# Optimization experiments

Hardware: AMD Instinct MI355X
Metric: run time of the kernel (lower is better)

## Reference

```python
import jax, jax.numpy as jnp
import numpy as np

E = 512
H = 8
D = E // H
HID = 2048
NE = 4
TOPK = 2
EPS = 1e-5
NEG = -1e9


def _ln(x, w, b):
    mu = jnp.mean(x, axis=-1, keepdims=True)
    var = jnp.mean(jnp.square(x - mu), axis=-1, keepdims=True)
    return (x - mu) * jax.lax.rsqrt(var + EPS) * w + b


def _expert(xf, mask, ln1_w, ln1_b, ipw, ipb, opw, opb, ln2_w, ln2_b, w1, b1, w2, b2):
    # xf: [T, E]; mask: [T] bool (allowed keys = routed tokens)
    T = xf.shape[0]
    h = _ln(xf, ln1_w, ln1_b)
    qkv = h @ ipw.T + ipb                       # [T, 3E]
    q, k, v = jnp.split(qkv, 3, axis=-1)
    q = q.reshape(T, H, D).transpose(1, 0, 2)   # [H, T, D]
    k = k.reshape(T, H, D).transpose(1, 0, 2)
    v = v.reshape(T, H, D).transpose(1, 0, 2)
    scores = jnp.einsum('htd,hsd->hts', q, k) / jnp.sqrt(jnp.asarray(D, xf.dtype))
    scores = jnp.where(mask[None, None, :], scores, NEG)
    a = jax.nn.softmax(scores, axis=-1)
    o = jnp.einsum('hts,hsd->htd', a, v).transpose(1, 0, 2).reshape(T, E)
    o = o @ opw.T + opb
    x1 = xf + o                                 # residual (dropout = identity, eval)
    h2 = _ln(x1, ln2_w, ln2_b)
    m = jax.nn.gelu(h2 @ w1.T + b1, approximate=False) @ w2.T + b2
    return x1 + m


def setup_inputs() -> dict:
    key = jax.random.key(0)
    ks = jax.random.split(key, 16)
    s = 0.02
    inp = {
        'x': jax.random.normal(ks[0], (4, 512, E), dtype=jnp.float32),
        'gate_w': jax.random.normal(ks[1], (NE, E), dtype=jnp.float32) * s,
        'gate_b': jnp.zeros((NE,), jnp.float32),
        'ln1_w': jnp.ones((NE, E), jnp.float32),
        'ln1_b': jnp.zeros((NE, E), jnp.float32),
        'in_proj_w': jax.random.normal(ks[2], (NE, 3 * E, E), dtype=jnp.float32) * s,
        'in_proj_b': jnp.zeros((NE, 3 * E), jnp.float32),
        'out_proj_w': jax.random.normal(ks[3], (NE, E, E), dtype=jnp.float32) * s,
        'out_proj_b': jnp.zeros((NE, E), jnp.float32),
        'ln2_w': jnp.ones((NE, E), jnp.float32),
        'ln2_b': jnp.zeros((NE, E), jnp.float32),
        'mlp_w1': jax.random.normal(ks[4], (NE, HID, E), dtype=jnp.float32) * s,
        'mlp_b1': jnp.zeros((NE, HID), jnp.float32),
        'mlp_w2': jax.random.normal(ks[5], (NE, E, HID), dtype=jnp.float32) * s,
        'mlp_b2': jnp.zeros((NE, E), jnp.float32),
    }
    return inp


def reference(x, gate_w, gate_b, ln1_w, ln1_b, in_proj_w, in_proj_b, out_proj_w,
              out_proj_b, ln2_w, ln2_b, mlp_w1, mlp_b1, mlp_w2, mlp_b2):
    B, N, _ = x.shape
    T = B * N
    xf = x.reshape(T, E)
    logits = xf @ gate_w.T + gate_b                      # [T, NE]
    topk_val, topk_idx = jax.lax.top_k(logits, TOPK)
    probs = jax.nn.softmax(topk_val, axis=-1)            # [T, TOPK]
    out = jnp.zeros_like(xf)
    for kk in range(TOPK):
        idx = topk_idx[:, kk]
        w = probs[:, kk][:, None]
        for e in range(NE):
            mask = idx == e
            eo = _expert(xf, mask,
                         ln1_w[e], ln1_b[e], in_proj_w[e], in_proj_b[e],
                         out_proj_w[e], out_proj_b[e], ln2_w[e], ln2_b[e],
                         mlp_w1[e], mlp_b1[e], mlp_w2[e], mlp_b2[e])
            out = out + jnp.where(mask[:, None], eo * w, 0.0)
    return out.reshape(B, N, E)
```

## Files before the change

### kernel.cpp

```cpp
#include <hip/hip_runtime.h>
#include <hip/hip_bf16.h>

#define T_TOK 2048
#define E_DIM 512
#define NHEAD 8
#define DHEAD 64
#define HID_D 2048
#define NEXP 4
#define NROW_ (2 * T_TOK)
#define VT_STRIDE 4352

typedef short short8 __attribute__((ext_vector_type(8)));
typedef float floatx4 __attribute__((ext_vector_type(4)));

__device__ __forceinline__ void gld16(const void* g, void* l) {
  __builtin_amdgcn_global_load_lds((const __attribute__((address_space(1))) void*)g,
                                   (__attribute__((address_space(3))) void*)l, 16, 0, 0);
}

__device__ inline float wave_sum(float v) {
  for (int off = 32; off > 0; off >>= 1) v += __shfl_xor(v, off);
  return v;
}

__device__ __forceinline__ unsigned pack_bf2(float a, float b) {
  __hip_bfloat16 ha = __float2bfloat16(a), hb = __float2bfloat16(b);
  unsigned ua = *(unsigned short*)&ha, ub = *(unsigned short*)&hb;
  return ua | (ub << 16);
}

__device__ __forceinline__ void cvt4(const float* __restrict__ s, __hip_bfloat16* __restrict__ d,
                                     int i4, int n) {
  if (i4 < n) {
    float4 v = *reinterpret_cast<const float4*>(s + i4);
    __hip_bfloat16 tmp[4] = {__float2bfloat16(v.x), __float2bfloat16(v.y),
                             __float2bfloat16(v.z), __float2bfloat16(v.w)};
    *reinterpret_cast<ushort4*>(d + i4) = *reinterpret_cast<const ushort4*>(tmp);
  }
}

__global__ void cvt_weights(const float* __restrict__ s0, const float* __restrict__ s1,
                            const float* __restrict__ s2, const float* __restrict__ s3,
                            __hip_bfloat16* d0, __hip_bfloat16* d1,
                            __hip_bfloat16* d2, __hip_bfloat16* d3,
                            int n0, int n1, int n2, int n3) {
  int i4 = (blockIdx.x * 256 + threadIdx.x) * 4;
  cvt4(s0, d0, i4, n0);
  cvt4(s1, d1, i4, n1);
  cvt4(s2, d2, i4, n2);
  cvt4(s3, d3, i4, n3);
}

__global__ void gate_kernel(const float* __restrict__ x, const float* __restrict__ gw,
                            const float* __restrict__ gb, int* token_e, float* token_p) {
  int wid = threadIdx.x >> 6, lane = threadIdx.x & 63;
  int t = blockIdx.x * 4 + wid;
  float a0 = 0, a1 = 0, a2 = 0, a3 = 0;
  for (int i = 0; i < 8; i++) {
    int c = lane + 64 * i;
    float xv = x[(size_t)t * E_DIM + c];
    a0 += xv * gw[0 * E_DIM + c];
    a1 += xv * gw[1 * E_DIM + c];
    a2 += xv * gw[2 * E_DIM + c];
    a3 += xv * gw[3 * E_DIM + c];
  }
  a0 = wave_sum(a0); a1 = wave_sum(a1); a2 = wave_sum(a2); a3 = wave_sum(a3);
  if (lane == 0) {
    float lg[4] = {a0 + gb[0], a1 + gb[1], a2 + gb[2], a3 + gb[3]};
    int i0 = 0;
    for (int e = 1; e < 4; e++) if (lg[e] > lg[i0]) i0 = e;
    int i1 = -1;
    for (int e = 0; e < 4; e++) {
      if (e == i0) continue;
      if (i1 < 0 || lg[e] > lg[i1]) i1 = e;
    }
    float e1 = __expf(lg[i1] - lg[i0]);
    float inv = 1.f / (1.f + e1);
    token_e[t] = i0; token_e[T_TOK + t] = i1;
    token_p[t] = inv; token_p[T_TOK + t] = e1 * inv;
  }
}

__global__ void count_kernel(const int* __restrict__ token_e, int* counts) {
  int g = blockIdx.x, kk = g >> 2, e = g & 3;
  __shared__ int ws4[4];
  int tid = threadIdx.x, wid = tid >> 6, lane = tid & 63;
  int c = 0;
  for (int t = tid; t < T_TOK; t += 256) c += (token_e[kk * T_TOK + t] == e);
  for (int off = 32; off; off >>= 1) c += __shfl_xor(c, off);
  if (lane == 0) ws4[wid] = c;
  __syncthreads();
  if (tid == 0) counts[g] = ws4[0] + ws4[1] + ws4[2] + ws4[3];
}

__global__ void offs_kernel(const int* __restrict__ counts, int* offs, int* padoffs) {
  int o = 0, po = 0;
  offs[0] = 0; padoffs[0] = 0;
  for (int g = 0; g < 8; g++) {
    o += counts[g]; offs[g + 1] = o;
    po += (counts[g] + 31) & ~31; padoffs[g + 1] = po;
  }
}

__global__ void compact_kernel(const int* __restrict__ token_e, const int* __restrict__ offs,
                               const int* __restrict__ padoffs, int* perm, int* rowg,
                               int* pmap, int* invrow) {
  int g = blockIdx.x, kk = g >> 2, e = g & 3;
  __shared__ int wcnt[4];
  __shared__ int base;
  int tid = threadIdx.x, wid = tid >> 6, lane = tid & 63;
  int og = offs[g], pg = padoffs[g];
  if (tid == 0) base = 0;
  __syncthreads();
  for (int t0 = 0; t0 < T_TOK; t0 += 256) {
    int t = t0 + tid;
    bool pred = token_e[kk * T_TOK + t] == e;
    unsigned long long mask = __ballot(pred);
    int rank = __popcll(mask & ((1ull << lane) - 1ull));
    if (lane == 0) wcnt[wid] = __popcll(mask);
    __syncthreads();
    int woff = 0;
    for (int i = 0; i < wid; i++) woff += wcnt[i];
    if (pred) {
      int row = og + base + woff + rank;
      perm[row] = t;
      rowg[row] = g;
      pmap[row] = pg + (row - og);
      invrow[kk * T_TOK + t] = row;
    }
    __syncthreads();
    if (tid == 0) base += wcnt[0] + wcnt[1] + wcnt[2] + wcnt[3];
    __syncthreads();
  }
}

__global__ void ln_kernel(const float* __restrict__ src, const int* __restrict__ perm,
                          const int* __restrict__ rowg, const float* __restrict__ lnw,
                          const float* __restrict__ lnb, __hip_bfloat16* __restrict__ dst) {
  int wid = threadIdx.x >> 6, lane = threadIdx.x & 63;
  int row = blockIdx.x * 4 + wid;
  int e = rowg[row] & 3;
  const float* xr = src + (size_t)(perm ? perm[row] : row) * E_DIM;
  float v[8];
  float s = 0;
  for (int i = 0; i < 8; i++) { v[i] = xr[lane + 64 * i]; s += v[i]; }
  s = wave_sum(s);
  float mu = s * (1.f / 512.f);
  float q = 0;
  for (int i = 0; i < 8; i++) { float d = v[i] - mu; q += d * d; }
  q = wave_sum(q);
  float rstd = rsqrtf(q * (1.f / 512.f) + 1e-5f);
  for (int i = 0; i < 8; i++) {
    int c = lane + 64 * i;
    dst[(size_t)row * E_DIM + c] =
        __float2bfloat16((v[i] - mu) * rstd * lnw[e * E_DIM + c] + lnb[e * E_DIM + c]);
  }
}

__global__ void transpose_v(const short* __restrict__ v, const int* __restrict__ pmap,
                            short* __restrict__ vT) {
  __shared__ short tile[64][65];
  int r0 = blockIdx.x * 64, c0 = blockIdx.y * 64;
  int tc = threadIdx.x & 63, tr4 = threadIdx.x >> 6;
  for (int i = 0; i < 64; i += 4)
    tile[tr4 + i][tc] = v[(size_t)(r0 + tr4 + i) * E_DIM + c0 + tc];
  __syncthreads();
  int pcol = pmap[r0 + tc];
  for (int i = 0; i < 64; i += 4)
    vT[(size_t)(c0 + tr4 + i) * VT_STRIDE + pcol] = tile[tc][tr4 + i];
}

__global__ void zero_gaps(const int* __restrict__ offs, const int* __restrict__ padoffs,
                          short* __restrict__ vT) {
  int g = blockIdx.x;
  int cnt = offs[g + 1] - offs[g];
  int gap = (padoffs[g + 1] - padoffs[g]) - cnt;
  if ((int)threadIdx.x < gap) {
    int col = padoffs[g] + cnt + threadIdx.x;
    for (int d = blockIdx.y; d < E_DIM; d += gridDim.y)
      vT[(size_t)d * VT_STRIDE + col] = 0;
  }
}

__global__ __launch_bounds__(256) void attn_mfma(
    const short* __restrict__ qb, const short* __restrict__ kb,
    const short* __restrict__ vT, const int* __restrict__ offs,
    const int* __restrict__ padoffs, __hip_bfloat16* __restrict__ ob) {
  int d0 = blockIdx.x;
  int g = d0 & 7;
  int rem = d0 >> 3;
  int h = rem >> 5;
  int qblk = rem & 31;
  int sbeg = offs[g], rend = offs[g + 1];
  int q0 = sbeg + qblk * 64;
  if (q0 >= rend) return;
  int G = rend - sbeg;
  int pg = padoffs[g];
  int tid = threadIdx.x, wid = tid >> 6, lane = tid & 63;
  int fr = lane & 15, lg = lane >> 4;
  int qw = q0 + wid * 16;

  __shared__ short Kt[2][32 * 64];
  __shared__ short Vt[2][64 * 32];

  int arow = qw + fr; if (arow > rend - 1) arow = rend - 1;
  const short* qp = qb + (size_t)arow * E_DIM + h * DHEAD;
  short8 qf0 = *reinterpret_cast<const short8*>(qp + lg * 8);
  short8 qf1 = *reinterpret_cast<const short8*>(qp + 32 + lg * 8);

  int offB = tid * 16;
  int krow = offB >> 7, kinner = offB & 127;
  int ksrc = (kinner ^ ((krow & 7) << 4)) >> 1;
  int vL = offB ^ (((offB >> 7) & 7) << 4);
  int vd = vL >> 6, vkey0 = (vL & 63) >> 1;
  int wb = wid * 512;
  const short* vrow = vT + (size_t)(h * DHEAD + vd) * VT_STRIDE + pg;

  auto stage = [&](int buf, int kbase) {
    int gr = sbeg + kbase + krow; if (gr > NROW_ - 1) gr = NROW_ - 1;
    gld16(kb + (size_t)gr * E_DIM + h * DHEAD + ksrc, &Kt[buf][wb]);
    gld16(vrow + kbase + vkey0, &Vt[buf][wb]);
  };

  floatx4 acc[4] = {};
  float m_r = -1e30f, l_r = 0.f;

  stage(0, 0);
  asm volatile("s_waitcnt vmcnt(0)" ::: "memory");
  __syncthreads();

  int cur = 0;
  for (int kbase = 0; kbase < G; kbase += 32) {
    if (kbase + 32 < G) stage(cur ^ 1, kbase + 32);
    const char* Kb = (const char*)&Kt[cur][0];
    const char* Vb = (const char*)&Vt[cur][0];

    int r0r = fr, r1r = 16 + fr;
    short8 kf00 = *reinterpret_cast<const short8*>(Kb + r0r * 128 + ((lg * 16) ^ ((r0r & 7) << 4)));
    short8 kf01 = *reinterpret_cast<const short8*>(Kb + r0r * 128 + ((64 + lg * 16) ^ ((r0r & 7) << 4)));
    short8 kf10 = *reinterpret_cast<const short8*>(Kb + r1r * 128 + ((lg * 16) ^ ((r1r & 7) << 4)));
    short8 kf11 = *reinterpret_cast<const short8*>(Kb + r1r * 128 + ((64 + lg * 16) ^ ((r1r & 7) << 4)));

    floatx4 s0 = {}, s1 = {};
    s0 = __builtin_amdgcn_mfma_f32_16x16x32_bf16(kf00, qf0, s0, 0, 0, 0);
    s0 = __builtin_amdgcn_mfma_f32_16x16x32_bf16(kf01, qf1, s0, 0, 0, 0);
    s1 = __builtin_amdgcn_mfma_f32_16x16x32_bf16(kf10, qf0, s1, 0, 0, 0);
    s1 = __builtin_amdgcn_mfma_f32_16x16x32_bf16(kf11, qf1, s1, 0, 0, 0);

    float sv[8];
    float mloc = -1e30f;
#pragma unroll
    for (int j = 0; j < 4; j++) {
      int k0 = kbase + lg * 4 + j;
      sv[j] = (k0 < G) ? s0[j] * 0.125f : -1e30f;
      sv[4 + j] = (k0 + 16 < G) ? s1[j] * 0.125f : -1e30f;
      mloc = fmaxf(mloc, fmaxf(sv[j], sv[4 + j]));
    }
    mloc = fmaxf(mloc, __shfl_xor(mloc, 16));
    mloc = fmaxf(mloc, __shfl_xor(mloc, 32));
    if (__any(mloc > m_r + 8.f)) {
      float mn = fmaxf(m_r, mloc);
      float corr = __expf(m_r - mn);
      m_r = mn;
      l_r *= corr;
      float cq0 = __shfl(corr, lg * 4 + 0), cq1 = __shfl(corr, lg * 4 + 1);
      float cq2 = __shfl(corr, lg * 4 + 2), cq3 = __shfl(corr, lg * 4 + 3);
#pragma unroll
      for (int db = 0; db < 4; db++) {
        acc[db][0] *= cq0; acc[db][1] *= cq1; acc[db][2] *= cq2; acc[db][3] *= cq3;
      }
    }
    float p[8], sl = 0.f;
#pragma unroll
    for (int i = 0; i < 8; i++) { p[i] = __expf(sv[i] - m_r); sl += p[i]; }
    sl += __shfl_xor(sl, 16);
    sl += __shfl_xor(sl, 32);
    l_r += sl;

    union { unsigned u[4]; short8 s8; } pa0, pa1;
    pa0.u[0] = pack_bf2(p[0], p[1]); pa0.u[1] = pack_bf2(p[2], p[3]);
    pa0.u[2] = 0; pa0.u[3] = 0;
    pa1.u[0] = pack_bf2(p[4], p[5]); pa1.u[1] = pack_bf2(p[6], p[7]);
    pa1.u[2] = 0; pa1.u[3] = 0;

#pragma unroll
    for (int db = 0; db < 4; db++) {
      int dd = db * 16 + fr;
      int s = ((dd >> 1) & 7) << 4;
      uint2 w0 = *reinterpret_cast<const uint2*>(Vb + ((dd * 64 + lg * 8) ^ s));
      uint2 w1 = *reinterpret_cast<const uint2*>(Vb + ((dd * 64 + 32 + lg * 8) ^ s));
      union { unsigned u[4]; short8 s8; } bv0, bv1;
      bv0.u[0] = w0.x; bv0.u[1] = w0.y; bv0.u[2] = 0; bv0.u[3] = 0;
      bv1.u[0] = w1.x; bv1.u[1] = w1.y; bv1.u[2] = 0; bv1.u[3] = 0;
      acc[db] = __builtin_amdgcn_mfma_f32_16x16x32_bf16(pa0.s8, bv0.s8, acc[db], 0, 0, 0);
      acc[db] = __builtin_amdgcn_mfma_f32_16x16x32_bf16(pa1.s8, bv1.s8, acc[db], 0, 0, 0);
    }

    asm volatile("s_waitcnt vmcnt(0)" ::: "memory");
    __syncthreads();
    cur ^= 1;
  }

  float lq0 = __shfl(l_r, lg * 4 + 0), lq1 = __shfl(l_r, lg * 4 + 1);
  float lq2 = __shfl(l_r, lg * 4 + 2), lq3 = __shfl(l_r, lg * 4 + 3);
  float lq[4] = {lq0, lq1, lq2, lq3};
#pragma unroll
  for (int db = 0; db < 4; db++)
#pragma unroll
    for (int j = 0; j < 4; j++) {
      int row = qw + lg * 4 + j;
      if (row < rend)
        ob[(size_t)row * E_DIM + h * DHEAD + db * 16 + fr] = __float2bfloat16(acc[db][j] / lq[j]);
    }
}

template <int MODE>
__global__ __launch_bounds__(256) void gemm_mfma(
    const short* __restrict__ A, const short* __restrict__ Wb,
    const float* __restrict__ bias, const int* __restrict__ offs,
    const int* __restrict__ perm, const float* __restrict__ resid,
    __hip_bfloat16* __restrict__ bq, __hip_bfloat16* __restrict__ bk,
    __hip_bfloat16* __restrict__ bv, float* __restrict__ outf) {
  constexpr int K = (MODE == 3) ? HID_D : E_DIM;
  constexpr int N = (MODE == 0) ? 3 * E_DIM : (MODE == 2) ? HID_D : E_DIM;
  constexpr int NKSTEP = K / 64;
  constexpr int NXB = 32;
  __shared__ short Abuf[2][4096];
  __shared__ short Bbuf[2][4096];

  int d = blockIdx.x;
  int g = d & 7;
  int rem = d >> 3;
  int yb = rem / NXB, xb = rem % NXB;
  int e = g & 3;
  int rbeg = offs[g], rend = offs[g + 1];
  int row0 = rbeg + xb * 64;
  if (row0 >= rend) return;
  int col0 = yb * 64;
  int tid = threadIdx.x;
  int wid = tid >> 6, lane = tid & 63;
  int wm = wid >> 1, wn = wid & 1;
  int fr = lane & 15, lg = lane >> 4;
  const short* wbase = Wb + (size_t)e * N * K;

  int st_row[2], st_src[2], st_arow[2];
  int wavebase = wid << 9;
  for (int c = 0; c < 2; c++) {
    int off = c * 4096 + tid * 16;
    int trow = off >> 7;
    int inner = off & 127;
    st_row[c] = trow;
    st_src[c] = (inner ^ ((trow & 7) << 4)) >> 1;
    int ga = row0 + trow;
    st_arow[c] = ga < rend ? ga : rend - 1;
  }

  auto stage = [&](int buf, int kb) {
#pragma unroll
    for (int c = 0; c < 2; c++) {
      gld16(A + (size_t)st_arow[c] * K + kb + st_src[c], &Abuf[buf][c * 2048 + wavebase]);
      gld16(wbase + (size_t)(col0 + st_row[c]) * K + kb + st_src[c],
            &Bbuf[buf][c * 2048 + wavebase]);
    }
  };

  floatx4 acc[2][2] = {};
  stage(0, 0);
  asm volatile("s_waitcnt vmcnt(0)" ::: "memory");
  __syncthreads();

  int cur = 0;
  for (int t = 0; t < NKSTEP; ++t) {
    if (t + 1 < NKSTEP) stage(cur ^ 1, (t + 1) * 64);
    const char* Ab = (const char*)&Abuf[cur][0];
    const char* Bb = (const char*)&Bbuf[cur][0];
    short8 af[2][2], bf8[2][2];
#pragma unroll
    for (int mi = 0; mi < 2; mi++)
#pragma unroll
      for (int ks = 0; ks < 2; ks++) {
        int row = wm * 32 + mi * 16 + fr;
        int cb = ks * 64 + lg * 16;
        af[mi][ks] = *reinterpret_cast<const short8*>(Ab + row * 128 + (cb ^ ((row & 7) << 4)));
      }
#pragma unroll
    for (int ni = 0; ni < 2; ni++)
#pragma unroll
      for (int ks = 0; ks < 2; ks++) {
        int row = wn * 32 + ni * 16 + fr;
        int cb = ks * 64 + lg * 16;
        bf8[ni][ks] = *reinterpret_cast<const short8*>(Bb + row * 128 + (cb ^ ((row & 7) << 4)));
      }
#pragma unroll
    for (int mi = 0; mi < 2; mi++)
#pragma unroll
      for (int ni = 0; ni < 2; ni++) {
        acc[mi][ni] = __builtin_amdgcn_mfma_f32_16x16x32_bf16(af[mi][0], bf8[ni][0], acc[mi][ni], 0, 0, 0);
        acc[mi][ni] = __builtin_amdgcn_mfma_f32_16x16x32_bf16(af[mi][1], bf8[ni][1], acc[mi][ni], 0, 0, 0);
      }
    asm volatile("s_waitcnt vmcnt(0)" ::: "memory");
    __syncthreads();
    cur ^= 1;
  }

  for (int mi = 0; mi < 2; mi++)
    for (int ni = 0; ni < 2; ni++)
      for (int j = 0; j < 4; j++) {
        int row = row0 + wm * 32 + mi * 16 + lg * 4 + j;
        if (row >= rend) continue;
        int col = col0 + wn * 32 + ni * 16 + fr;
        float val = acc[mi][ni][j] + bias[e * N + col];
        if constexpr (MODE == 0) {
          if (col < E_DIM) bq[(size_t)row * E_DIM + col] = __float2bfloat16(val);
          else if (col < 2 * E_DIM) bk[(size_t)row * E_DIM + col - E_DIM] = __float2bfloat16(val);
          else bv[(size_t)row * E_DIM + col - 2 * E_DIM] = __float2bfloat16(val);
        } else if constexpr (MODE == 1) {
          int t = perm[row];
          outf[(size_t)row * E_DIM + col] = val + resid[(size_t)t * E_DIM + col];
        } else if constexpr (MODE == 2) {
          float gl = 0.5f * val * (1.f + erff(val * 0.70710678118654752f));
          bq[(size_t)row * HID_D + col] = __float2bfloat16(gl);
        } else {
          outf[(size_t)row * E_DIM + col] = val + resid[(size_t)row * E_DIM + col];
        }
      }
}

__global__ void combine_kernel(const float* __restrict__ y, const int* __restrict__ invrow,
                               const float* __restrict__ token_p, float* __restrict__ out) {
  int t = blockIdx.x;
  int r0 = invrow[t], r1 = invrow[T_TOK + t];
  float p0 = token_p[t], p1 = token_p[T_TOK + t];
  const float* y0 = y + (size_t)r0 * E_DIM;
  const float* y1 = y + (size_t)r1 * E_DIM;
  float* o = out + (size_t)t * E_DIM;
  for (int i = threadIdx.x; i < E_DIM; i += 256) o[i] = p0 * y0[i] + p1 * y1[i];
}

extern "C" void kernel_launch(void* const* d_in, const int* in_sizes, int n_in,
                              void* d_out, int out_size, void* d_ws, size_t ws_size,
                              hipStream_t stream) {
  const float* x      = (const float*)d_in[0];
  const float* gate_w = (const float*)d_in[1];
  const float* gate_b = (const float*)d_in[2];
  const float* ln1_w  = (const float*)d_in[3];
  const float* ln1_b  = (const float*)d_in[4];
  const float* ipw    = (const float*)d_in[5];
  const float* ipb    = (const float*)d_in[6];
  const float* opw    = (const float*)d_in[7];
  const float* opb    = (const float*)d_in[8];
  const float* ln2_w  = (const float*)d_in[9];
  const float* ln2_b  = (const float*)d_in[10];
  const float* w1     = (const float*)d_in[11];
  const float* b1     = (const float*)d_in[12];
  const float* w2     = (const float*)d_in[13];
  const float* b2     = (const float*)d_in[14];
  float* out = (float*)d_out;

  const int SZ_IP = NEXP * 3 * E_DIM * E_DIM;
  const int SZ_OP = NEXP * E_DIM * E_DIM;
  const int SZ_W1 = NEXP * HID_D * E_DIM;
  const int SZ_W2 = NEXP * E_DIM * HID_D;
  const int NROW = NROW_;

  char* ws = (char*)d_ws;
  size_t off = 0;
  auto carve = [&](size_t bytes) -> void* {
    void* p = ws + off;
    off += (bytes + 255) & ~(size_t)255;
    return p;
  };
  __hip_bfloat16* ipw_bf = (__hip_bfloat16*)carve((size_t)SZ_IP * 2);
  __hip_bfloat16* opw_bf = (__hip_bfloat16*)carve((size_t)SZ_OP * 2);
  __hip_bfloat16* w1_bf  = (__hip_bfloat16*)carve((size_t)SZ_W1 * 2);
  __hip_bfloat16* w2_bf  = (__hip_bfloat16*)carve((size_t)SZ_W2 * 2);
  __hip_bfloat16* h_bf   = (__hip_bfloat16*)carve((size_t)NROW * E_DIM * 2);
  __hip_bfloat16* q_bf   = (__hip_bfloat16*)carve((size_t)NROW * E_DIM * 2);
  __hip_bfloat16* k_bf   = (__hip_bfloat16*)carve((size_t)NROW * E_DIM * 2);
  __hip_bfloat16* v_bf   = (__hip_bfloat16*)carve((size_t)NROW * E_DIM * 2);
  __hip_bfloat16* o_bf   = (__hip_bfloat16*)carve((size_t)NROW * E_DIM * 2);
  __hip_bfloat16* h2_bf  = (__hip_bfloat16*)carve((size_t)NROW * E_DIM * 2);
  __hip_bfloat16* mid_bf = (__hip_bfloat16*)carve((size_t)NROW * HID_D * 2);
  short* vT     = (short*)carve((size_t)E_DIM * VT_STRIDE * 2);
  float* x1     = (float*)carve((size_t)NROW * E_DIM * 4);
  int* token_e  = (int*)carve((size_t)NROW * 4);
  float* token_p= (float*)carve((size_t)NROW * 4);
  int* perm     = (int*)carve((size_t)NROW * 4);
  int* rowg     = (int*)carve((size_t)NROW * 4);
  int* pmap     = (int*)carve((size_t)NROW * 4);
  int* invrow   = (int*)carve((size_t)NROW * 4);
  int* counts   = (int*)carve(8 * 4);
  int* offs     = (int*)carve(9 * 4);
  int* padoffs  = (int*)carve(9 * 4);
  float* ybuf = (float*)h_bf;

  cvt_weights<<<SZ_W1 / 4 / 256, 256, 0, stream>>>(ipw, opw, w1, w2, ipw_bf, opw_bf,
                                                   w1_bf, w2_bf, SZ_IP, SZ_OP, SZ_W1, SZ_W2);
  gate_kernel<<<T_TOK / 4, 256, 0, stream>>>(x, gate_w, gate_b, token_e, token_p);
  count_kernel<<<8, 256, 0, stream>>>(token_e, counts);
  offs_kernel<<<1, 1, 0, stream>>>(counts, offs, padoffs);
  compact_kernel<<<8, 256, 0, stream>>>(token_e, offs, padoffs, perm, rowg, pmap, invrow);
  ln_kernel<<<NROW / 4, 256, 0, stream>>>(x, perm, rowg, ln1_w, ln1_b, h_bf);
  gemm_mfma<0><<<8 * 24 * 32, 256, 0, stream>>>((const short*)h_bf, (const short*)ipw_bf,
      ipb, offs, perm, nullptr, q_bf, k_bf, v_bf, nullptr);
  transpose_v<<<dim3(NROW / 64, E_DIM / 64), 256, 0, stream>>>((const short*)v_bf, pmap, vT);
  zero_gaps<<<dim3(8, 64), 32, 0, stream>>>(offs, padoffs, vT);
  attn_mfma<<<8 * 8 * 32, 256, 0, stream>>>((const short*)q_bf, (const short*)k_bf,
      vT, offs, padoffs, o_bf);
  gemm_mfma<1><<<8 * 8 * 32, 256, 0, stream>>>((const short*)o_bf, (const short*)opw_bf,
      opb, offs, perm, x, nullptr, nullptr, nullptr, x1);
  ln_kernel<<<NROW / 4, 256, 0, stream>>>(x1, nullptr, rowg, ln2_w, ln2_b, h2_bf);
  gemm_mfma<2><<<8 * 32 * 32, 256, 0, stream>>>((const short*)h2_bf, (const short*)w1_bf,
      b1, offs, perm, nullptr, mid_bf, nullptr, nullptr, nullptr);
  gemm_mfma<3><<<8 * 8 * 32, 256, 0, stream>>>((const short*)mid_bf, (const short*)w2_bf,
      b2, offs, perm, x1, nullptr, nullptr, nullptr, ybuf);
  combine_kernel<<<T_TOK, 256, 0, stream>>>(ybuf, invrow, token_p, out);
  (void)in_sizes; (void)n_in; (void)ws_size;
}
```

Measured before the change: 189.8 us.

## Split-K the MLP down-projection and triple-buffer GEMM staging

The MODE 3 GEMM (K=2048) is split into two K halves, doubling its grid. The second half writes partial sums to a separate buffer that reuses the k/v scratch space, and combine_kernel adds the two partials. All GEMM modes now use three LDS stages with two loads in flight, waiting on vmcnt(4) rather than draining every step. This aims to fill more CUs on the long-K GEMM and hide global-load latency, at the cost of extra partial-sum memory traffic and 1.5x LDS per block, which may lower occupancy.

```diff
diff --git a/kernel.cpp b/kernel.cpp
--- a/kernel.cpp
+++ b/kernel.cpp
@@ -320,23 +320,29 @@
     const float* __restrict__ bias, const int* __restrict__ offs,
     const int* __restrict__ perm, const float* __restrict__ resid,
     __hip_bfloat16* __restrict__ bq, __hip_bfloat16* __restrict__ bk,
-    __hip_bfloat16* __restrict__ bv, float* __restrict__ outf) {
+    __hip_bfloat16* __restrict__ bv, float* __restrict__ outf,
+    float* __restrict__ outf2) {
   constexpr int K = (MODE == 3) ? HID_D : E_DIM;
   constexpr int N = (MODE == 0) ? 3 * E_DIM : (MODE == 2) ? HID_D : E_DIM;
-  constexpr int NKSTEP = K / 64;
+  constexpr bool SPLIT = (MODE == 3);
+  constexpr int KLEN = SPLIT ? K / 2 : K;
+  constexpr int NKSTEP = KLEN / 64;
   constexpr int NXB = 32;
-  __shared__ short Abuf[2][4096];
-  __shared__ short Bbuf[2][4096];
+  __shared__ short Abuf[3][4096];
+  __shared__ short Bbuf[3][4096];
 
   int d = blockIdx.x;
   int g = d & 7;
   int rem = d >> 3;
+  int ksel = 0;
+  if constexpr (SPLIT) { ksel = rem & 1; rem >>= 1; }
   int yb = rem / NXB, xb = rem % NXB;
   int e = g & 3;
   int rbeg = offs[g], rend = offs[g + 1];
   int row0 = rbeg + xb * 64;
   if (row0 >= rend) return;
   int col0 = yb * 64;
+  int kbeg = ksel * KLEN;
   int tid = threadIdx.x;
   int wid = tid >> 6, lane = tid & 63;
   int wm = wid >> 1, wn = wid & 1;
@@ -365,15 +371,18 @@
   };
 
   floatx4 acc[2][2] = {};
-  stage(0, 0);
-  asm volatile("s_waitcnt vmcnt(0)" ::: "memory");
-  __syncthreads();
-
-  int cur = 0;
+  stage(0, kbeg);
+  stage(1, kbeg + 64);
+  asm volatile("s_waitcnt vmcnt(4)" ::: "memory");
+  __builtin_amdgcn_s_barrier();
+  __builtin_amdgcn_sched_barrier(0);
+
+  int bcur = 0;
   for (int t = 0; t < NKSTEP; ++t) {
-    if (t + 1 < NKSTEP) stage(cur ^ 1, (t + 1) * 64);
-    const char* Ab = (const char*)&Abuf[cur][0];
-    const char* Bb = (const char*)&Bbuf[cur][0];
+    int b2 = bcur + 2; if (b2 >= 3) b2 -= 3;
+    if (t + 2 < NKSTEP) stage(b2, kbeg + (t + 2) * 64);
+    const char* Ab = (const char*)&Abuf[bcur][0];
+    const char* Bb = (const char*)&Bbuf[bcur][0];
     short8 af[2][2], bf8[2][2];
 #pragma unroll
     for (int mi = 0; mi < 2; mi++)
@@ -398,9 +407,14 @@
         acc[mi][ni] = __builtin_amdgcn_mfma_f32_16x16x32_bf16(af[mi][0], bf8[ni][0], acc[mi][ni], 0, 0, 0);
         acc[mi][ni] = __builtin_amdgcn_mfma_f32_16x16x32_bf16(af[mi][1], bf8[ni][1], acc[mi][ni], 0, 0, 0);
       }
-    asm volatile("s_waitcnt vmcnt(0)" ::: "memory");
-    __syncthreads();
-    cur ^= 1;
+    if (t + 1 < NKSTEP) {
+      if (t + 2 < NKSTEP) asm volatile("s_waitcnt vmcnt(4)" ::: "memory");
+      else                asm volatile("s_waitcnt vmcnt(0)" ::: "memory");
+      asm volatile("s_waitcnt lgkmcnt(0)" ::: "memory");
+      __builtin_amdgcn_s_barrier();
+      __builtin_amdgcn_sched_barrier(0);
+    }
+    bcur = (bcur + 1 == 3) ? 0 : bcur + 1;
   }
 
   for (int mi = 0; mi < 2; mi++)
@@ -409,7 +423,8 @@
         int row = row0 + wm * 32 + mi * 16 + lg * 4 + j;
         if (row >= rend) continue;
         int col = col0 + wn * 32 + ni * 16 + fr;
-        float val = acc[mi][ni][j] + bias[e * N + col];
+        float val = acc[mi][ni][j];
+        if constexpr (MODE != 3) val += bias[e * N + col];
         if constexpr (MODE == 0) {
           if (col < E_DIM) bq[(size_t)row * E_DIM + col] = __float2bfloat16(val);
           else if (col < 2 * E_DIM) bk[(size_t)row * E_DIM + col - E_DIM] = __float2bfloat16(val);
@@ -421,20 +436,29 @@
           float gl = 0.5f * val * (1.f + erff(val * 0.70710678118654752f));
           bq[(size_t)row * HID_D + col] = __float2bfloat16(gl);
         } else {
-          outf[(size_t)row * E_DIM + col] = val + resid[(size_t)row * E_DIM + col];
+          if (ksel == 0) {
+            val += bias[e * N + col] + resid[(size_t)row * E_DIM + col];
+            outf[(size_t)row * E_DIM + col] = val;
+          } else {
+            outf2[(size_t)row * E_DIM + col] = val;
+          }
         }
       }
 }
 
-__global__ void combine_kernel(const float* __restrict__ y, const int* __restrict__ invrow,
+__global__ void combine_kernel(const float* __restrict__ y1, const float* __restrict__ y2,
+                               const int* __restrict__ invrow,
                                const float* __restrict__ token_p, float* __restrict__ out) {
   int t = blockIdx.x;
   int r0 = invrow[t], r1 = invrow[T_TOK + t];
   float p0 = token_p[t], p1 = token_p[T_TOK + t];
-  const float* y0 = y + (size_t)r0 * E_DIM;
-  const float* y1 = y + (size_t)r1 * E_DIM;
+  const float* a0 = y1 + (size_t)r0 * E_DIM;
+  const float* b0 = y2 + (size_t)r0 * E_DIM;
+  const float* a1 = y1 + (size_t)r1 * E_DIM;
+  const float* b1 = y2 + (size_t)r1 * E_DIM;
   float* o = out + (size_t)t * E_DIM;
-  for (int i = threadIdx.x; i < E_DIM; i += 256) o[i] = p0 * y0[i] + p1 * y1[i];
+  for (int i = threadIdx.x; i < E_DIM; i += 256)
+    o[i] = p0 * (a0[i] + b0[i]) + p1 * (a1[i] + b1[i]);
 }
 
 extern "C" void kernel_launch(void* const* d_in, const int* in_sizes, int n_in,
@@ -492,7 +516,8 @@
   int* counts   = (int*)carve(8 * 4);
   int* offs     = (int*)carve(9 * 4);
   int* padoffs  = (int*)carve(9 * 4);
-  float* ybuf = (float*)h_bf;
+  float* ybuf  = (float*)h_bf;
+  float* ybuf2 = (float*)k_bf;
 
   cvt_weights<<<SZ_W1 / 4 / 256, 256, 0, stream>>>(ipw, opw, w1, w2, ipw_bf, opw_bf,
                                                    w1_bf, w2_bf, SZ_IP, SZ_OP, SZ_W1, SZ_W2);
@@ -502,18 +527,18 @@
   compact_kernel<<<8, 256, 0, stream>>>(token_e, offs, padoffs, perm, rowg, pmap, invrow);
   ln_kernel<<<NROW / 4, 256, 0, stream>>>(x, perm, rowg, ln1_w, ln1_b, h_bf);
   gemm_mfma<0><<<8 * 24 * 32, 256, 0, stream>>>((const short*)h_bf, (const short*)ipw_bf,
-      ipb, offs, perm, nullptr, q_bf, k_bf, v_bf, nullptr);
+      ipb, offs, perm, nullptr, q_bf, k_bf, v_bf, nullptr, nullptr);
   transpose_v<<<dim3(NROW / 64, E_DIM / 64), 256, 0, stream>>>((const short*)v_bf, pmap, vT);
   zero_gaps<<<dim3(8, 64), 32, 0, stream>>>(offs, padoffs, vT);
   attn_mfma<<<8 * 8 * 32, 256, 0, stream>>>((const short*)q_bf, (const short*)k_bf,
       vT, offs, padoffs, o_bf);
   gemm_mfma<1><<<8 * 8 * 32, 256, 0, stream>>>((const short*)o_bf, (const short*)opw_bf,
-      opb, offs, perm, x, nullptr, nullptr, nullptr, x1);
+      opb, offs, perm, x, nullptr, nullptr, nullptr, x1, nullptr);
   ln_kernel<<<NROW / 4, 256, 0, stream>>>(x1, nullptr, rowg, ln2_w, ln2_b, h2_bf);
   gemm_mfma<2><<<8 * 32 * 32, 256, 0, stream>>>((const short*)h2_bf, (const short*)w1_bf,
-      b1, offs, perm, nullptr, mid_bf, nullptr, nullptr, nullptr);
-  gemm_mfma<3><<<8 * 8 * 32, 256, 0, stream>>>((const short*)mid_bf, (const short*)w2_bf,
-      b2, offs, perm, x1, nullptr, nullptr, nullptr, ybuf);
-  combine_kernel<<<T_TOK, 256, 0, stream>>>(ybuf, invrow, token_p, out);
+      b1, offs, perm, nullptr, mid_bf, nullptr, nullptr, nullptr, nullptr);
+  gemm_mfma<3><<<8 * 2 * 8 * 32, 256, 0, stream>>>((const short*)mid_bf, (const short*)w2_bf,
+      b2, offs, perm, x1, nullptr, nullptr, nullptr, ybuf, ybuf2);
+  combine_kernel<<<T_TOK, 256, 0, stream>>>(ybuf, ybuf2, invrow, token_p, out);
   (void)in_sizes; (void)n_in; (void)ws_size;
 }
```

Result: faster. 183.6 us (-3.2%).
